# Performance work log

Measured on AMD Instinct MI355X. Metric: run time of the kernel, lower is better.

The kernel has to match this reference:

```python
import jax, jax.numpy as jnp
import numpy as np

N_EMBD = 1024
N_HEADS = 16
HEAD_DIM = N_EMBD // N_HEADS


def setup_inputs() -> dict:
    key = jax.random.key(0)
    k0, k1, k2, k3, k4 = jax.random.split(key, 5)
    scale = 1.0 / np.sqrt(N_EMBD)
    x = jax.random.normal(k0, (2, 2048, N_EMBD), dtype=jnp.float32)
    # nn.Linear(n_embd, 3*n_embd): weight [3d, d], bias [3d]
    w_qkv = jax.random.normal(k1, (3 * N_EMBD, N_EMBD), dtype=jnp.float32) * scale
    b_qkv = jax.random.normal(k2, (3 * N_EMBD,), dtype=jnp.float32) * scale
    w_proj = jax.random.normal(k3, (N_EMBD, N_EMBD), dtype=jnp.float32) * scale
    b_proj = jax.random.normal(k4, (N_EMBD,), dtype=jnp.float32) * scale
    return {"x": x, "w_qkv": w_qkv, "b_qkv": b_qkv, "w_proj": w_proj, "b_proj": b_proj}


def reference(x, w_qkv, b_qkv, w_proj, b_proj):
    b, l, d = x.shape
    h, f = N_HEADS, HEAD_DIM
    qkv = x @ w_qkv.T + b_qkv                      # [b, l, 3d]
    # rearrange 'b l (c h f) -> c b h l f'
    qkv = qkv.reshape(b, l, 3, h, f)
    q = jnp.transpose(qkv[:, :, 0], (0, 2, 1, 3))  # [b, h, l, f]
    k = jnp.transpose(qkv[:, :, 1], (0, 2, 1, 3))
    v = jnp.transpose(qkv[:, :, 2], (0, 2, 1, 3))
    scores = jnp.einsum('bhqf,bhkf->bhqk', q, k) / jnp.sqrt(jnp.float32(f))
    att = jax.nn.softmax(scores, axis=-1)          # [b, h, l, l]
    y = jnp.einsum('bhqk,bhkf->bhqf', att, v)      # [b, h, l, f]
    y = jnp.transpose(y, (0, 2, 1, 3)).reshape(b, l, d)  # 'b h l f -> b l (h f)'
    return y @ w_proj.T + b_proj
```

## Files before the change

### kernel.cpp

```cpp
#include <hip/hip_runtime.h>
#include <hip/hip_bf16.h>
#include <stdint.h>


typedef unsigned short u16;
typedef __attribute__((ext_vector_type(8))) short short8;
typedef __attribute__((ext_vector_type(4))) float f32x4;
typedef __attribute__((ext_vector_type(16))) float f32x16;
typedef __attribute__((ext_vector_type(4))) unsigned int u32x4;

#define MFMA16(a, b, c) __builtin_amdgcn_mfma_f32_16x16x32_bf16((a), (b), (c), 0, 0, 0)
#define MFMA32(a, b, c) __builtin_amdgcn_mfma_f32_32x32x16_bf16((a), (b), (c), 0, 0, 0)

__device__ __forceinline__ u16 f2bf(float x) {
  union { float f; uint32_t u; } v; v.f = x;
  uint32_t r = v.u + 0x7FFFu + ((v.u >> 16) & 1u);
  return (u16)(r >> 16);
}

__device__ __forceinline__ float fexp2(float x) {
#if __has_builtin(__builtin_amdgcn_exp2f)
  return __builtin_amdgcn_exp2f(x);
#else
  return exp2f(x);
#endif
}

__device__ __forceinline__ uint32_t pkbf(float lo, float hi) {
  uint32_t a = __builtin_bit_cast(uint32_t, lo) + 0x8000u;
  uint32_t b = __builtin_bit_cast(uint32_t, hi) + 0x8000u;
  return __builtin_amdgcn_perm(b, a, 0x07060302u);
}

__device__ __forceinline__ uint32_t cvtpk(float lo, float hi) {
  uint32_t r;
  asm("v_cvt_pk_bf16_f32 %0, %1, %2" : "=v"(r) : "v"(lo), "v"(hi));
  return r;
}

__device__ __forceinline__ void gload16(const void* g, void* l) {
  __builtin_amdgcn_global_load_lds((const __attribute__((address_space(1))) void*)g,
                                   (__attribute__((address_space(3))) void*)l, 16, 0, 0);
}

__global__ __launch_bounds__(256) void cvt_all(const float* __restrict__ x,
                                               const float* __restrict__ wq,
                                               const float* __restrict__ wp,
                                               u16* __restrict__ xb,
                                               u16* __restrict__ wqb,
                                               u16* __restrict__ wpb) {
  int i = blockIdx.x * 256 + threadIdx.x;
  const float* s; u16* d; int off;
  if (i < 1048576) { s = x; d = xb; off = i; }
  else if (i < 1835008) { s = wq; d = wqb; off = i - 1048576; }
  else { s = wp; d = wpb; off = i - 1835008; }
  float4 f = reinterpret_cast<const float4*>(s)[off];
  ushort4 o;
  o.x = f2bf(f.x); o.y = f2bf(f.y); o.z = f2bf(f.z); o.w = f2bf(f.w);
  reinterpret_cast<ushort4*>(d)[off] = o;
}

template <int EPI>
__global__ __launch_bounds__(256, 4) void gemm_bt(const u16* __restrict__ A,
                                                  const u16* __restrict__ B,
                                                  const float* __restrict__ bias,
                                                  u16* __restrict__ outb,
                                                  float* __restrict__ outf,
                                                  int M, int N, int K) {
  __shared__ u16 smem[16384];
  const int tid = threadIdx.x;
  const int lane = tid & 63;
  const int wid = tid >> 6;
  const int bn = blockIdx.x, bm = blockIdx.y;
  const int row0 = bm * 128, col0 = bn * 128;
  const int wr = wid >> 1, wc = wid & 1;
  const int fr = lane & 15, fq = lane >> 4;

  f32x4 acc[4][4];
  #pragma unroll
  for (int m = 0; m < 4; m++)
    #pragma unroll
    for (int n = 0; n < 4; n++)
      #pragma unroll
      for (int j = 0; j < 4; j++) acc[m][n][j] = 0.f;

  const int cB = tid + 256;
  const int rA1 = tid >> 2, rA2 = cB >> 2;
  const int lA1 = (tid & 3) ^ ((tid >> 3) & 3);
  const int lA2 = (cB & 3) ^ ((cB >> 3) & 3);
  const size_t ga1 = (size_t)rA1 * K + lA1 * 8;
  const size_t ga2 = (size_t)rA2 * K + lA2 * 8;
  const int d1 = tid * 8, d2 = cB * 8;
  const u16* Ab = A + (size_t)row0 * K;
  const u16* Bb = B + (size_t)col0 * K;

  const int sl = (fq ^ ((fr >> 1) & 3)) * 8;
  const int niter = K >> 5;

  {
    u16* s = smem;
    gload16(Ab + ga1, s + d1);
    gload16(Ab + ga2, s + d2);
    gload16(Bb + ga1, s + 4096 + d1);
    gload16(Bb + ga2, s + 4096 + d2);
  }
  __syncthreads();

  for (int t = 0; t < niter; t++) {
    if (t + 1 < niter) {
      u16* s = smem + ((t + 1) & 1) * 8192;
      const size_t k0 = (size_t)(t + 1) * 32;
      gload16(Ab + ga1 + k0, s + d1);
      gload16(Ab + ga2 + k0, s + d2);
      gload16(Bb + ga1 + k0, s + 4096 + d1);
      gload16(Bb + ga2 + k0, s + 4096 + d2);
    }
    const u16* sa = smem + (t & 1) * 8192;
    const u16* sb = sa + 4096;
    short8 a[4], b[4];
    #pragma unroll
    for (int m = 0; m < 4; m++)
      a[m] = *(const short8*)&sa[(wr * 64 + m * 16 + fr) * 32 + sl];
    #pragma unroll
    for (int n = 0; n < 4; n++)
      b[n] = *(const short8*)&sb[(wc * 64 + n * 16 + fr) * 32 + sl];
    __builtin_amdgcn_s_setprio(1);
    #pragma unroll
    for (int m = 0; m < 4; m++)
      #pragma unroll
      for (int n = 0; n < 4; n++)
        acc[m][n] = MFMA16(a[m], b[n], acc[m][n]);
    __builtin_amdgcn_s_setprio(0);
    __syncthreads();
  }

  if (EPI == 0) {
    if (bn < 16) {
      #pragma unroll
      for (int m = 0; m < 4; m++) {
        #pragma unroll
        for (int n = 0; n < 4; n++) {
          #pragma unroll
          for (int j = 0; j < 4; j++) {
            int r = row0 + wr * 64 + m * 16 + fq * 4 + j;
            int c = col0 + wc * 64 + n * 16 + fr;
            float v = acc[m][n][j] + bias[c];
            int d = c & 1023, h = d >> 6, f = d & 63;
            int bb = r >> 11, ll = r & 2047;
            int bhh = bb * 16 + h;
            if (bn < 8) {
              outb[((size_t)bhh * 2048 + ll) * 64 + f] = f2bf(v * 0.18033688f);
            } else {
              outb[4194304u + ((size_t)bhh * 2048 + ll) * 64 + f] = f2bf(v);
            }
          }
        }
      }
    } else {
      u16* sC = smem;
      #pragma unroll
      for (int m = 0; m < 4; m++) {
        #pragma unroll
        for (int n = 0; n < 4; n++) {
          int c_local = wc * 64 + n * 16 + fr;
          int r_base = wr * 64 + m * 16 + fq * 4;
          float bi = bias[col0 + c_local];
          uint2 w;
          w.x = pkbf(acc[m][n][0] + bi, acc[m][n][1] + bi);
          w.y = pkbf(acc[m][n][2] + bi, acc[m][n][3] + bi);
          *(uint2*)&sC[c_local * 128 + (r_base ^ ((c_local & 7) << 3))] = w;
        }
      }
      __syncthreads();
      const int h0 = (col0 - 2048) >> 6;
      const int ll0 = row0 & 2047;
      const int bb = row0 >> 11;
      #pragma unroll
      for (int it = 0; it < 8; it++) {
        int chunk = tid + it * 256;
        int row_c = chunk >> 4, off = chunk & 15;
        short8 v = *(const short8*)&sC[row_c * 128 + ((off * 8) ^ ((row_c & 7) << 3))];
        int h = h0 + (row_c >> 6), f = row_c & 63;
        *(short8*)&outb[8388608u + ((size_t)((bb * 16 + h) * 64 + f)) * 2048 + ll0 + off * 8] = v;
      }
    }
  } else {
    #pragma unroll
    for (int m = 0; m < 4; m++)
      #pragma unroll
      for (int n = 0; n < 4; n++)
        #pragma unroll
        for (int j = 0; j < 4; j++) {
          int r = row0 + wr * 64 + m * 16 + fq * 4 + j;
          int c = col0 + wc * 64 + n * 16 + fr;
          outf[(size_t)r * N + c] = acc[m][n][j] + bias[c];
        }
  }
}

__device__ __forceinline__ void softpack1(const f32x16& st, float& lp,
                                          short8& paA, short8& paB) {
  float e[16];
  #pragma unroll
  for (int r = 0; r < 16; r++) e[r] = fexp2(st[r]);
  float s0 = (e[0] + e[1]) + (e[2] + e[3]);
  float s1 = (e[4] + e[5]) + (e[6] + e[7]);
  float s2 = (e[8] + e[9]) + (e[10] + e[11]);
  float s3 = (e[12] + e[13]) + (e[14] + e[15]);
  lp += (s0 + s1) + (s2 + s3);
  #pragma unroll
  for (int cc = 0; cc < 2; cc++) {
    uint32_t g0 = cvtpk(e[8 * cc + 0], e[8 * cc + 1]);
    uint32_t g1 = cvtpk(e[8 * cc + 2], e[8 * cc + 3]);
    uint32_t g2 = cvtpk(e[8 * cc + 4], e[8 * cc + 5]);
    uint32_t g3 = cvtpk(e[8 * cc + 6], e[8 * cc + 7]);
    asm volatile("v_permlane32_swap_b32 %0, %1" : "+v"(g0), "+v"(g2));
    asm volatile("v_permlane32_swap_b32 %0, %1" : "+v"(g1), "+v"(g3));
    u32x4 t;
    t[0] = g0; t[1] = g1; t[2] = g2; t[3] = g3;
    if (cc == 0) paA = __builtin_bit_cast(short8, t);
    else paB = __builtin_bit_cast(short8, t);
  }
}

__global__ __launch_bounds__(512, 4) void attn_kernel(const u16* __restrict__ qg,
                                                      const u16* __restrict__ kg,
                                                      const u16* __restrict__ vtg,
                                                      u16* __restrict__ y) {
  __shared__ u16 sStage[24576];
  __shared__ float sL2[128];
  const int x = blockIdx.x;
  const int bh = (x & 7) * 4 + (x >> 7);
  const int qt = (x >> 3) & 15;
  const int tid = threadIdx.x, l = tid & 63, wid = tid >> 6;
  const int qs = wid & 3, kh = wid >> 2;
  const int col = l & 31, hi = l >> 5;
  const size_t base = (size_t)bh * 131072;
  const u16* qp = qg + base;
  const int qrow = qt * 128 + qs * 32;

  short8 qf[4];
  #pragma unroll
  for (int kk = 0; kk < 4; kk++)
    qf[kk] = *(const short8*)&qp[(size_t)(qrow + col) * 64 + kk * 16 + hi * 8];

  const bool isK = tid < 256;
  int srcoff, dstoff;
  if (isK) {
    int cc = tid, row = cc >> 3;
    srcoff = row * 64 + (((cc & 7) ^ (row & 7)) * 8);
    dstoff = cc * 8;
  } else {
    int cv = tid - 256, row = cv >> 2;
    srcoff = row * 2048 + (((cv & 3) ^ ((cv >> 3) & 3)) * 8);
    dstoff = 2048 + cv * 8;
  }
  u16* R0 = sStage;
  u16* R1 = sStage + 12288;
  const u16* kbase0 = kg + base;
  const u16* kbase1 = kg + base + 65536;
  const u16* vbase0 = vtg + base;
  const u16* vbase1 = vtg + base + 1024;

  f32x16 o0, o1, zv;
  float lp = 0.f;
  #pragma unroll
  for (int r = 0; r < 16; r++) { o0[r] = 0.f; o1[r] = 0.f; zv[r] = 0.f; }

  const int krsw = (col & 7) << 3;
  const int vrsw = ((col >> 1) & 3) << 3;
  const u16* Rw = sStage + kh * 12288;

  auto STAGE = [&](int tt, int buf) {
    if (isK) {
      gload16(kbase0 + (size_t)tt * 2048 + srcoff, R0 + buf * 4096 + dstoff);
      gload16(kbase1 + (size_t)tt * 2048 + srcoff, R1 + buf * 4096 + dstoff);
    } else {
      gload16(vbase0 + tt * 32 + srcoff, R0 + buf * 4096 + dstoff);
      gload16(vbase1 + tt * 32 + srcoff, R1 + buf * 4096 + dstoff);
    }
  };

  STAGE(0, 0);
  int sel = 0;
  for (int t = 0; t < 32; t++) {
    const int nb = (sel == 2) ? 0 : sel + 1;
    if (t + 1 < 32) {
      STAGE(t + 1, nb);
      asm volatile("s_waitcnt vmcnt(2)" ::: "memory");
    } else {
      asm volatile("s_waitcnt vmcnt(0)" ::: "memory");
    }
    __builtin_amdgcn_s_barrier();
    __builtin_amdgcn_sched_barrier(0);
    const u16* S = Rw + sel * 4096;

    f32x16 st;
    __builtin_amdgcn_s_setprio(1);
    {
      short8 kb = *(const short8*)&S[col * 64 + ((hi * 8) ^ krsw)];
      st = MFMA32(kb, qf[0], zv);
    }
    #pragma unroll
    for (int kk = 1; kk < 4; kk++) {
      short8 kb = *(const short8*)&S[col * 64 + ((kk * 16 + hi * 8) ^ krsw)];
      st = MFMA32(kb, qf[kk], st);
    }
    __builtin_amdgcn_s_setprio(0);

    short8 pa[2];
    softpack1(st, lp, pa[0], pa[1]);

    __builtin_amdgcn_s_setprio(1);
    #pragma unroll
    for (int c = 0; c < 2; c++) {
      short8 vb0 = *(const short8*)&S[2048 + col * 32 + ((c * 16 + hi * 8) ^ vrsw)];
      short8 vb1 = *(const short8*)&S[2048 + (32 + col) * 32 + ((c * 16 + hi * 8) ^ vrsw)];
      o0 = MFMA32(pa[c], vb0, o0);
      o1 = MFMA32(pa[c], vb1, o1);
    }
    __builtin_amdgcn_s_setprio(0);
    sel = nb;
  }

  __syncthreads();
  float* sM = (float*)sStage;
  float* sMl = sM + 8192;
  if (kh == 1) {
    #pragma unroll
    for (int r = 0; r < 16; r++) {
      sM[qs * 2048 + r * 64 + l] = o0[r];
      sM[qs * 2048 + (16 + r) * 64 + l] = o1[r];
    }
    sMl[qs * 64 + l] = lp;
  }
  __syncthreads();
  if (kh == 0) {
    #pragma unroll
    for (int r = 0; r < 16; r++) {
      o0[r] += sM[qs * 2048 + r * 64 + l];
      o1[r] += sM[qs * 2048 + (16 + r) * 64 + l];
    }
    lp += sMl[qs * 64 + l];
    float lsum = lp + __shfl_xor(lp, 32);
    if (l < 32) sL2[qs * 32 + col] = 1.0f / lsum;
    __builtin_amdgcn_s_waitcnt(0);
    const int b = bh >> 4, hh = bh & 15;
    #pragma unroll
    for (int fvt = 0; fvt < 2; fvt++) {
      #pragma unroll
      for (int r = 0; r < 16; r++) {
        int q = (r & 3) + 8 * (r >> 2) + 4 * hi;
        float li = sL2[qs * 32 + q];
        float v = (fvt == 0 ? o0[r] : o1[r]) * li;
        y[((size_t)(b * 2048 + qrow + q)) * 1024 + hh * 64 + fvt * 32 + col] = f2bf(v);
      }
    }
  }
}

extern "C" void kernel_launch(void* const* d_in, const int* in_sizes, int n_in,
                              void* d_out, int out_size, void* d_ws, size_t ws_size,
                              hipStream_t stream) {
  const float* x = (const float*)d_in[0];
  const float* w_qkv = (const float*)d_in[1];
  const float* b_qkv = (const float*)d_in[2];
  const float* w_proj = (const float*)d_in[3];
  const float* b_proj = (const float*)d_in[4];
  float* out = (float*)d_out;

  u16* ws = (u16*)d_ws;
  u16* xb = ws;
  u16* wq = xb + 4194304;
  u16* wp = wq + 3145728;
  u16* qb = wp + 1048576;
  u16* kb = qb + 4194304;
  u16* vb = kb + 4194304;
  u16* yb = vb + 4194304;

  cvt_all<<<8192, 256, 0, stream>>>(x, w_qkv, w_proj, xb, wq, wp);

  gemm_bt<0><<<dim3(24, 32), 256, 0, stream>>>(xb, wq, b_qkv, qb, nullptr, 4096, 3072, 1024);

  attn_kernel<<<512, 512, 0, stream>>>(qb, kb, vb, yb);

  gemm_bt<1><<<dim3(8, 32), 256, 0, stream>>>(yb, wp, b_proj, nullptr, out, 4096, 1024, 1024);
}
```

Measured before the change: 113.2 us.

## Process two KV tiles per iteration with a four-buffer LDS ring

Grows the LDS staging ring from three to four buffers per half and restructures the main loop to handle two key/value tiles per barrier. The loads for the next pair are issued after the barrier, and both QK products are computed before the softmax and PV steps. This halves the number of barriers and waits and gives the scheduler more independent MFMA work to overlap with exp/pack. In exchange, shared memory use rises, which may limit occupancy, and the full vmcnt(0) wait exposes load latency at the start of each pair.

New measurement: 114.5 us. About the same (+1.2%).

```diff
diff --git a/kernel.cpp b/kernel.cpp
--- a/kernel.cpp
+++ b/kernel.cpp
@@ -227,7 +227,7 @@
                                                       const u16* __restrict__ kg,
                                                       const u16* __restrict__ vtg,
                                                       u16* __restrict__ y) {
-  __shared__ u16 sStage[24576];
+  __shared__ u16 sStage[32768];
   __shared__ float sL2[128];
   const int x = blockIdx.x;
   const int bh = (x & 7) * 4 + (x >> 7);
@@ -256,7 +256,7 @@
     dstoff = 2048 + cv * 8;
   }
   u16* R0 = sStage;
-  u16* R1 = sStage + 12288;
+  u16* R1 = sStage + 16384;
   const u16* kbase0 = kg + base;
   const u16* kbase1 = kg + base + 65536;
   const u16* vbase0 = vtg + base;
@@ -269,9 +269,10 @@
 
   const int krsw = (col & 7) << 3;
   const int vrsw = ((col >> 1) & 3) << 3;
-  const u16* Rw = sStage + kh * 12288;
-
-  auto STAGE = [&](int tt, int buf) {
+  const u16* Rw = sStage + kh * 16384;
+
+  auto STAGE = [&](int tt) {
+    const int buf = tt & 3;
     if (isK) {
       gload16(kbase0 + (size_t)tt * 2048 + srcoff, R0 + buf * 4096 + dstoff);
       gload16(kbase1 + (size_t)tt * 2048 + srcoff, R1 + buf * 4096 + dstoff);
@@ -281,20 +282,7 @@
     }
   };
 
-  STAGE(0, 0);
-  int sel = 0;
-  for (int t = 0; t < 32; t++) {
-    const int nb = (sel == 2) ? 0 : sel + 1;
-    if (t + 1 < 32) {
-      STAGE(t + 1, nb);
-      asm volatile("s_waitcnt vmcnt(2)" ::: "memory");
-    } else {
-      asm volatile("s_waitcnt vmcnt(0)" ::: "memory");
-    }
-    __builtin_amdgcn_s_barrier();
-    __builtin_amdgcn_sched_barrier(0);
-    const u16* S = Rw + sel * 4096;
-
+  auto QK = [&](const u16* S) -> f32x16 {
     f32x16 st;
     __builtin_amdgcn_s_setprio(1);
     {
@@ -307,10 +295,10 @@
       st = MFMA32(kb, qf[kk], st);
     }
     __builtin_amdgcn_s_setprio(0);
-
-    short8 pa[2];
-    softpack1(st, lp, pa[0], pa[1]);
-
+    return st;
+  };
+
+  auto PV = [&](const u16* S, short8* pa) {
     __builtin_amdgcn_s_setprio(1);
     #pragma unroll
     for (int c = 0; c < 2; c++) {
@@ -320,7 +308,25 @@
       o1 = MFMA32(pa[c], vb1, o1);
     }
     __builtin_amdgcn_s_setprio(0);
-    sel = nb;
+  };
+
+  STAGE(0);
+  STAGE(1);
+  for (int t = 0; t < 32; t += 2) {
+    asm volatile("s_waitcnt vmcnt(0)" ::: "memory");
+    __builtin_amdgcn_s_barrier();
+    __builtin_amdgcn_sched_barrier(0);
+    if (t + 2 < 32) STAGE(t + 2);
+    if (t + 3 < 32) STAGE(t + 3);
+    const u16* SA = Rw + (t & 3) * 4096;
+    const u16* SB = Rw + ((t + 1) & 3) * 4096;
+    f32x16 stA = QK(SA);
+    f32x16 stB = QK(SB);
+    short8 pa[2], pb[2];
+    softpack1(stA, lp, pa[0], pa[1]);
+    PV(SA, pa);
+    softpack1(stB, lp, pb[0], pb[1]);
+    PV(SB, pb);
   }
 
   __syncthreads();
```

## Stage 64-key tiles with double buffering and half as many barriers

Applied to the files above, without the earlier changes.

The attention kernel now loads 64 keys per pipeline step, two 32-key sub-tiles, instead of 32. The K/V staging ring changes from triple to double buffering, with each thread issuing four global-to-LDS loads per stage. The loop runs 16 iterations with one wait-and-barrier each instead of 32, which cuts sync overhead and lengthens the window in which loads overlap compute. In exchange LDS use grows to 64KB, which may reduce occupancy. The wait now comes after compute, so prefetch depth is one stage.

New measurement: 112.6 us (median of 2 runs). No clear change (-0.5%).

```diff
diff --git a/kernel.cpp b/kernel.cpp
--- a/kernel.cpp
+++ b/kernel.cpp
@@ -227,7 +227,7 @@
                                                       const u16* __restrict__ kg,
                                                       const u16* __restrict__ vtg,
                                                       u16* __restrict__ y) {
-  __shared__ u16 sStage[24576];
+  __shared__ u16 sStage[32768];
   __shared__ float sL2[128];
   const int x = blockIdx.x;
   const int bh = (x & 7) * 4 + (x >> 7);
@@ -245,85 +245,85 @@
     qf[kk] = *(const short8*)&qp[(size_t)(qrow + col) * 64 + kk * 16 + hi * 8];
 
   const bool isK = tid < 256;
-  int srcoff, dstoff;
-  if (isK) {
-    int cc = tid, row = cc >> 3;
-    srcoff = row * 64 + (((cc & 7) ^ (row & 7)) * 8);
-    dstoff = cc * 8;
-  } else {
-    int cv = tid - 256, row = cv >> 2;
-    srcoff = row * 2048 + (((cv & 3) ^ ((cv >> 3) & 3)) * 8);
-    dstoff = 2048 + cv * 8;
+  const int ca = isK ? tid : (tid - 256);
+  const int cb = ca + 256;
+  int srcA, srcB, dstA, dstB;
+  {
+    int rA = ca >> 3, rB = cb >> 3;
+    int rowstride = isK ? 64 : 2048;
+    srcA = rA * rowstride + (((ca & 7) ^ (rA & 7)) * 8);
+    srcB = rB * rowstride + (((cb & 7) ^ (rB & 7)) * 8);
+    dstA = (isK ? 0 : 4096) + ca * 8;
+    dstB = (isK ? 0 : 4096) + cb * 8;
   }
   u16* R0 = sStage;
-  u16* R1 = sStage + 12288;
-  const u16* kbase0 = kg + base;
-  const u16* kbase1 = kg + base + 65536;
-  const u16* vbase0 = vtg + base;
-  const u16* vbase1 = vtg + base + 1024;
+  u16* R1 = sStage + 16384;
+  const u16* gb0 = isK ? (kg + base) : (vtg + base);
+  const u16* gb1 = isK ? (kg + base + 65536) : (vtg + base + 1024);
 
   f32x16 o0, o1, zv;
   float lp = 0.f;
   #pragma unroll
   for (int r = 0; r < 16; r++) { o0[r] = 0.f; o1[r] = 0.f; zv[r] = 0.f; }
 
-  const int krsw = (col & 7) << 3;
-  const int vrsw = ((col >> 1) & 3) << 3;
-  const u16* Rw = sStage + kh * 12288;
+  const int rsw = (col & 7) << 3;
+  const u16* Rw = sStage + kh * 16384;
 
   auto STAGE = [&](int tt, int buf) {
-    if (isK) {
-      gload16(kbase0 + (size_t)tt * 2048 + srcoff, R0 + buf * 4096 + dstoff);
-      gload16(kbase1 + (size_t)tt * 2048 + srcoff, R1 + buf * 4096 + dstoff);
-    } else {
-      gload16(vbase0 + tt * 32 + srcoff, R0 + buf * 4096 + dstoff);
-      gload16(vbase1 + tt * 32 + srcoff, R1 + buf * 4096 + dstoff);
-    }
+    const size_t toff = isK ? (size_t)tt * 4096 : (size_t)tt * 64;
+    gload16(gb0 + toff + srcA, R0 + buf * 8192 + dstA);
+    gload16(gb1 + toff + srcA, R1 + buf * 8192 + dstA);
+    gload16(gb0 + toff + srcB, R0 + buf * 8192 + dstB);
+    gload16(gb1 + toff + srcB, R1 + buf * 8192 + dstB);
   };
 
   STAGE(0, 0);
+  asm volatile("s_waitcnt vmcnt(0)" ::: "memory");
+  __builtin_amdgcn_s_barrier();
+  __builtin_amdgcn_sched_barrier(0);
+
   int sel = 0;
-  for (int t = 0; t < 32; t++) {
-    const int nb = (sel == 2) ? 0 : sel + 1;
-    if (t + 1 < 32) {
-      STAGE(t + 1, nb);
-      asm volatile("s_waitcnt vmcnt(2)" ::: "memory");
-    } else {
-      asm volatile("s_waitcnt vmcnt(0)" ::: "memory");
-    }
+  for (int t = 0; t < 16; t++) {
+    const int nb = sel ^ 1;
+    if (t + 1 < 16) STAGE(t + 1, nb);
+    const u16* S = Rw + sel * 8192;
+
+    #pragma unroll
+    for (int sub = 0; sub < 2; sub++) {
+      const u16* Ks = S + sub * 2048;
+      f32x16 st;
+      __builtin_amdgcn_s_setprio(1);
+      {
+        short8 kb = *(const short8*)&Ks[col * 64 + ((hi * 8) ^ rsw)];
+        st = MFMA32(kb, qf[0], zv);
+      }
+      #pragma unroll
+      for (int kk = 1; kk < 4; kk++) {
+        short8 kb = *(const short8*)&Ks[col * 64 + ((kk * 16 + hi * 8) ^ rsw)];
+        st = MFMA32(kb, qf[kk], st);
+      }
+      __builtin_amdgcn_s_setprio(0);
+
+      short8 pa[2];
+      softpack1(st, lp, pa[0], pa[1]);
+
+      __builtin_amdgcn_s_setprio(1);
+      #pragma unroll
+      for (int c = 0; c < 2; c++) {
+        short8 vb0 = *(const short8*)&S[4096 + col * 64 + ((sub * 32 + c * 16 + hi * 8) ^ rsw)];
+        short8 vb1 = *(const short8*)&S[4096 + (32 + col) * 64 + ((sub * 32 + c * 16 + hi * 8) ^ rsw)];
+        o0 = MFMA32(pa[c], vb0, o0);
+        o1 = MFMA32(pa[c], vb1, o1);
+      }
+      __builtin_amdgcn_s_setprio(0);
+    }
+
+    asm volatile("s_waitcnt vmcnt(0)" ::: "memory");
     __builtin_amdgcn_s_barrier();
     __builtin_amdgcn_sched_barrier(0);
-    const u16* S = Rw + sel * 4096;
-
-    f32x16 st;
-    __builtin_amdgcn_s_setprio(1);
-    {
-      short8 kb = *(const short8*)&S[col * 64 + ((hi * 8) ^ krsw)];
-      st = MFMA32(kb, qf[0], zv);
-    }
-    #pragma unroll
-    for (int kk = 1; kk < 4; kk++) {
-      short8 kb = *(const short8*)&S[col * 64 + ((kk * 16 + hi * 8) ^ krsw)];
-      st = MFMA32(kb, qf[kk], st);
-    }
-    __builtin_amdgcn_s_setprio(0);
-
-    short8 pa[2];
-    softpack1(st, lp, pa[0], pa[1]);
-
-    __builtin_amdgcn_s_setprio(1);
-    #pragma unroll
-    for (int c = 0; c < 2; c++) {
-      short8 vb0 = *(const short8*)&S[2048 + col * 32 + ((c * 16 + hi * 8) ^ vrsw)];
-      short8 vb1 = *(const short8*)&S[2048 + (32 + col) * 32 + ((c * 16 + hi * 8) ^ vrsw)];
-      o0 = MFMA32(pa[c], vb0, o0);
-      o1 = MFMA32(pa[c], vb1, o1);
-    }
-    __builtin_amdgcn_s_setprio(0);
     sel = nb;
   }
 
-  __syncthreads();
   float* sM = (float*)sStage;
   float* sMl = sM + 8192;
   if (kh == 1) {
```
